# Kernel tuning notes

Measured on AMD Instinct MI355X. Metric: run time of the kernel, lower is better.

Reference implementation:

```python
import jax, jax.numpy as jnp
import numpy as np

B, C, S = 2048, 128, 10          # nodes, channels, species
DIN = 9                           # irreps dim of 0e+1o+2e
DOUTS = (1, 3, 5)                 # dims of output irreps 0e, 1o, 2e
PATHS = (1, 3, 8)                 # num CG paths per correlation order 1..3


def _sparse_normal(key, shape, density=0.15):
    kv, km = jax.random.split(key)
    v = jax.random.normal(kv, shape, jnp.float32)
    m = jax.random.uniform(km, shape) < density
    return jnp.where(m, v, 0.0)


def setup_inputs() -> dict:
    key = jax.random.key(0)
    ks = jax.random.split(key, 11)
    node_feats = jax.random.normal(ks[0], (B, C, DIN), jnp.float32)
    species = jax.random.randint(ks[1], (B,), 0, S)
    node_attrs = jax.nn.one_hot(species, S, dtype=jnp.float32)
    sc = jax.random.normal(ks[2], (B, C * DIN), jnp.float32)
    # CG "U" buffers, stacked over the 3 output irreps, d_out padded to 5.
    U1 = _sparse_normal(ks[3], (3, 5, DIN, PATHS[0]))
    U2 = _sparse_normal(ks[4], (3, 5, DIN, DIN, PATHS[1]))
    U3 = _sparse_normal(ks[5], (3, 5, DIN, DIN, DIN, PATHS[2]))
    # per-species path weights [l_out, species, paths, channels]
    W1 = jax.random.normal(ks[6], (3, S, PATHS[0], C), jnp.float32)
    W2 = jax.random.normal(ks[7], (3, S, PATHS[1], C), jnp.float32)
    W3 = jax.random.normal(ks[8], (3, S, PATHS[2], C), jnp.float32)
    # e3nn Linear: block-diagonal channel mixing per output irrep
    Wlin = jax.random.normal(ks[9], (3, C, C), jnp.float32)
    return dict(node_feats=node_feats, node_attrs=node_attrs, sc=sc,
                U1=U1, U2=U2, U3=U3, W1=W1, W2=W2, W3=W3, Wlin=Wlin)


def reference(node_feats, node_attrs, sc, U1, U2, U3, W1, W2, W3, Wlin):
    x = node_feats                                  # [B, C, 9]
    inv_sqrt_c = 1.0 / np.sqrt(C).astype(np.float32)
    outs = []
    for l, d in enumerate(DOUTS):                   # structural loop over output irreps
        # per-node, per-species weights: [B, P, C]
        w3 = jnp.einsum('be,epc->bpc', node_attrs, W3[l])
        w2 = jnp.einsum('be,epc->bpc', node_attrs, W2[l])
        w1 = jnp.einsum('be,epc->bpc', node_attrs, W1[l])
        u3, u2, u1 = U3[l, :d], U2[l, :d], U1[l, :d]
        # MACE recursive symmetric contraction (highest order first)
        out = jnp.einsum('mijkp,bpc,bck->bcmij', u3, w3, x)   # [B,C,d,9,9]
        out = out + jnp.einsum('mijp,bpc->bcmij', u2, w2)
        out = jnp.einsum('bcmij,bcj->bcmi', out, x)           # [B,C,d,9]
        out = out + jnp.einsum('mip,bpc->bcmi', u1, w1)
        out = jnp.einsum('bcmi,bci->bcm', out, x)             # [B,C,d]
        # axis_to_mul + e3nn Linear (per-irrep channel mixing, element path norm)
        y = jnp.einsum('bcm,cd->bdm', out, Wlin[l]) * inv_sqrt_c
        outs.append(y.reshape(y.shape[0], -1))                # [B, C*d]
    return jnp.concatenate(outs, axis=-1) + sc                # [B, 1152]
```

## Files before the change

kernel.cpp:

```cpp
#include <hip/hip_runtime.h>


#define NB 2048
#define NC 128
#define NS 10

__host__ __device__ constexpr int pidx(int j, int k) {
    return 9 * j - j * (j - 1) / 2 + (k - j);
}

struct TripTab {
    int ti[165], tj[165], tk[165];
    constexpr TripTab() : ti{}, tj{}, tk{} {
        int n = 0;
        for (int i = 0; i < 9; i++)
            for (int j = i; j < 9; j++)
                for (int k = j; k < 9; k++) { ti[n] = i; tj[n] = j; tk[n] = k; n++; }
    }
};
static constexpr TripTab TT{};

struct PairTab {
    int pj[45], pk[45];
    constexpr PairTab() : pj{}, pk{} {
        int n = 0;
        for (int j = 0; j < 9; j++)
            for (int k = j; k < 9; k++) { pj[n] = j; pk[n] = k; n++; }
    }
};
static constexpr PairTab PT{};

__global__ __launch_bounds__(256) void prep_kernel(const float* __restrict__ attrs,
                                                   int* __restrict__ cnt,
                                                   int* __restrict__ start,
                                                   int* __restrict__ list)
{
    __shared__ int sc_[256][NS];
    __shared__ int own_[256][NS];
    __shared__ int st_[NS];
    const int t = threadIdx.x;
    int myspec[8];
    #pragma unroll
    for (int e = 0; e < NS; e++) own_[t][e] = 0;
    #pragma unroll
    for (int r = 0; r < 8; r++) {
        const int b = t * 8 + r;
        const float* row = attrs + b * NS;
        int e = 0;
        #pragma unroll
        for (int s = 1; s < NS; s++) e = (row[s] > 0.5f) ? s : e;
        myspec[r] = e;
        own_[t][e] += 1;
    }
    #pragma unroll
    for (int e = 0; e < NS; e++) sc_[t][e] = own_[t][e];
    __syncthreads();
    for (int off = 1; off < 256; off <<= 1) {
        int tmp[NS];
        #pragma unroll
        for (int e = 0; e < NS; e++) tmp[e] = (t >= off) ? sc_[t - off][e] : 0;
        __syncthreads();
        #pragma unroll
        for (int e = 0; e < NS; e++) sc_[t][e] += tmp[e];
        __syncthreads();
    }
    if (t == 0) {
        int run = 0;
        for (int e = 0; e < NS; e++) {
            st_[e] = run; start[e] = run; cnt[e] = sc_[255][e]; run += sc_[255][e];
        }
    }
    __syncthreads();
    #pragma unroll
    for (int r = 0; r < 8; r++) {
        const int e = myspec[r];
        int rank = 0;
        #pragma unroll
        for (int r2 = 0; r2 < r; r2++) rank += (myspec[r2] == e) ? 1 : 0;
        const int pos = st_[e] + (sc_[t][e] - own_[t][e]) + rank;
        list[pos] = t * 8 + r;
    }
}

__global__ __launch_bounds__(256) void sym_kernel(const float* __restrict__ U2,
                                                  const float* __restrict__ U3,
                                                  float* __restrict__ U3sym,
                                                  float* __restrict__ U2sym)
{
    const int lm = blockIdx.x;
    const int t = threadIdx.x;
    if (t < 165) {
        const int i = TT.ti[t], j = TT.tj[t], k = TT.tk[t];
        const bool eab = (i == j), ebc = (j == k);
        float s[8] = {0, 0, 0, 0, 0, 0, 0, 0};
        auto addp = [&](int a, int b, int c) {
            const float* q = U3 + (((size_t)lm * 729) + a * 81 + b * 9 + c) * 8;
            #pragma unroll
            for (int p = 0; p < 8; p++) s[p] += q[p];
        };
        addp(i, j, k);
        if (!ebc)          addp(i, k, j);
        if (!eab)          addp(j, i, k);
        if (!eab)          addp(j, k, i);
        if (!ebc)          addp(k, i, j);
        if (!(eab || ebc)) addp(k, j, i);
        float* o = U3sym + ((size_t)lm * 165 + t) * 8;
        #pragma unroll
        for (int p = 0; p < 8; p++) o[p] = s[p];
    } else if (t < 210) {
        const int pp = t - 165;
        const int j = PT.pj[pp], k = PT.pk[pp];
        const float* a = U2 + ((size_t)lm * 81 + j * 9 + k) * 3;
        float v0 = a[0], v1 = a[1], v2 = a[2];
        if (j != k) {
            const float* b2 = U2 + ((size_t)lm * 81 + k * 9 + j) * 3;
            v0 += b2[0]; v1 += b2[1]; v2 += b2[2];
        }
        float* o = U2sym + ((size_t)lm * 45 + pp) * 3;
        o[0] = v0; o[1] = v1; o[2] = v2;
    }
}

__global__ __launch_bounds__(256) void main_kernel(
    const float* __restrict__ x_in,
    const float* __restrict__ U1,
    const float* __restrict__ U3sym, const float* __restrict__ U2sym,
    const float* __restrict__ W1, const float* __restrict__ W2, const float* __restrict__ W3,
    const int* __restrict__ cnt, const int* __restrict__ start, const int* __restrict__ list,
    float* __restrict__ inter)
{
    const int c = blockIdx.x;
    const int e = blockIdx.y;
    const int count = cnt[e];
    const int sbase = start[e];

    __shared__ __align__(16) float stab[9 * 660];
    __shared__ float w3s[3][8];
    __shared__ float w2s[3][3];
    __shared__ float w1s[3];

    const int t = threadIdx.x;
    if (t < 24)      { int l = t / 8, p = t % 8; w3s[l][p] = W3[((l * NS + e) * 8 + p) * NC + c]; }
    else if (t < 33) { int q = t - 24; int l = q / 3, p = q % 3; w2s[l][p] = W2[((l * NS + e) * 3 + p) * NC + c]; }
    else if (t < 36) { int l = t - 33; w1s[l] = W1[(l * NS + e) * NC + c]; }
    __syncthreads();

    {
        const int TB[9] = {0, 45, 81, 109, 130, 145, 155, 161, 164};
        for (int n = t; n < 495; n += 256) {
            const int mm = n / 55;
            const int s = n - mm * 55;
            int l, lm;
            if (mm == 0) { l = 0; lm = 0; } else if (mm < 4) { l = 1; lm = 4 + mm; } else { l = 2; lm = 6 + mm; }
            float* tb = stab + mm * 660;
            if (s < 45) {
                const int i = PT.pj[s], j = PT.pk[s];
                const int jj = j - i;
                const int t0 = TB[i] + (9 - i) * jj - jj * (jj - 1) / 2;
                for (int u = 0; u < 12; u++) {
                    float val = 0.f;
                    if (u < 9 - j) {
                        const float* a = U3sym + ((size_t)lm * 165 + t0 + u) * 8;
                        const float4 A = *(const float4*)a;
                        const float4 Bv = *(const float4*)(a + 4);
                        val = A.x * w3s[l][0];
                        val = fmaf(A.y,  w3s[l][1], val);
                        val = fmaf(A.z,  w3s[l][2], val);
                        val = fmaf(A.w,  w3s[l][3], val);
                        val = fmaf(Bv.x, w3s[l][4], val);
                        val = fmaf(Bv.y, w3s[l][5], val);
                        val = fmaf(Bv.z, w3s[l][6], val);
                        val = fmaf(Bv.w, w3s[l][7], val);
                    }
                    tb[s * 12 + u] = val;
                }
            } else if (s < 54) {
                const int j = s - 45;
                for (int u = 0; u < 12; u++) {
                    float val = 0.f;
                    if (u < 9 - j) {
                        const int pp = pidx(j, j + u);
                        const float* a = U2sym + ((size_t)lm * 45 + pp) * 3;
                        val = fmaf(a[0], w2s[l][0], fmaf(a[1], w2s[l][1], a[2] * w2s[l][2]));
                    }
                    tb[540 + j * 12 + u] = val;
                }
            } else {
                for (int u = 0; u < 12; u++) {
                    float val = (u < 9) ? U1[lm * 9 + u] * w1s[l] : 0.f;
                    tb[648 + u] = val;
                }
            }
        }
    }
    __syncthreads();

    #pragma unroll 1
    for (int idx = t; idx < count; idx += 256) {
        const int slot = sbase + idx;
        const int b = list[slot];
        const float* xp = x_in + ((size_t)b * NC + c) * 9;
        float x[9];
        #pragma unroll
        for (int k = 0; k < 9; k++) x[k] = xp[k];

        float* op = inter + ((size_t)c * NB + slot) * 12;

        #pragma unroll 1
        for (int mm = 0; mm < 9; mm++) {
            const float* bp = stab + mm * 660;
            float acc = 0.f;
            #pragma unroll
            for (int i = 0; i < 9; i++) {
                float acci = 0.f;
                #pragma unroll
                for (int j = i; j < 9; j++) {
                    const float* r = bp + pidx(i, j) * 12;
                    const int L = 9 - j;
                    const float4 q0 = *(const float4*)r;
                    float inner = q0.x * x[j];
                    if (L > 1) inner = fmaf(q0.y, x[j + 1], inner);
                    if (L > 2) inner = fmaf(q0.z, x[j + 2], inner);
                    if (L > 3) inner = fmaf(q0.w, x[j + 3], inner);
                    if (L > 4) {
                        const float4 q1 = *(const float4*)(r + 4);
                        inner = fmaf(q1.x, x[j + 4], inner);
                        if (L > 5) inner = fmaf(q1.y, x[j + 5], inner);
                        if (L > 6) inner = fmaf(q1.z, x[j + 6], inner);
                        if (L > 7) inner = fmaf(q1.w, x[j + 7], inner);
                        if (L > 8) {
                            const float4 q2 = *(const float4*)(r + 8);
                            inner = fmaf(q2.x, x[j + 8], inner);
                        }
                    }
                    acci = fmaf(x[j], inner, acci);
                }
                acc = fmaf(x[i], acci, acc);
            }
            #pragma unroll
            for (int j = 0; j < 9; j++) {
                const float* r = bp + 540 + j * 12;
                const int L = 9 - j;
                const float4 q0 = *(const float4*)r;
                float inner = q0.x * x[j];
                if (L > 1) inner = fmaf(q0.y, x[j + 1], inner);
                if (L > 2) inner = fmaf(q0.z, x[j + 2], inner);
                if (L > 3) inner = fmaf(q0.w, x[j + 3], inner);
                if (L > 4) {
                    const float4 q1 = *(const float4*)(r + 4);
                    inner = fmaf(q1.x, x[j + 4], inner);
                    if (L > 5) inner = fmaf(q1.y, x[j + 5], inner);
                    if (L > 6) inner = fmaf(q1.z, x[j + 6], inner);
                    if (L > 7) inner = fmaf(q1.w, x[j + 7], inner);
                    if (L > 8) {
                        const float4 q2 = *(const float4*)(r + 8);
                        inner = fmaf(q2.x, x[j + 8], inner);
                    }
                }
                acc = fmaf(x[j], inner, acc);
            }
            {
                const float* r = bp + 648;
                const float4 q0 = *(const float4*)r;
                const float4 q1 = *(const float4*)(r + 4);
                float inner = q0.x * x[0];
                inner = fmaf(q0.y, x[1], inner);
                inner = fmaf(q0.z, x[2], inner);
                inner = fmaf(q0.w, x[3], inner);
                inner = fmaf(q1.x, x[4], inner);
                inner = fmaf(q1.y, x[5], inner);
                inner = fmaf(q1.z, x[6], inner);
                inner = fmaf(q1.w, x[7], inner);
                inner = fmaf(r[8], x[8], inner);
                acc += inner;
            }
            op[mm] = acc;
        }
    }
}

__global__ __launch_bounds__(256) void final_kernel(
    const float* __restrict__ inter, const float* __restrict__ Wlin,
    const float* __restrict__ sc, const int* __restrict__ list,
    float* __restrict__ out)
{
    __shared__ float sInter[4 * NC * 12];
    const int t = threadIdx.x;
    const int s0 = blockIdx.x * 4;
    #pragma unroll
    for (int q = 0; q < 6; q++) {
        const int flat = t + q * 256;
        const int q3 = flat % 3;
        const int cs = flat / 3;
        const int cc = cs >> 2, s = cs & 3;
        const float4 v = *(const float4*)(inter + ((size_t)cc * NB + s0 + s) * 12 + q3 * 4);
        *(float4*)(&sInter[(s * NC + cc) * 12 + q3 * 4]) = v;
    }
    __syncthreads();

    const int dd = t & 127;
    const int bh = t >> 7;
    float acc[2][9];
    #pragma unroll
    for (int u = 0; u < 2; u++)
        #pragma unroll
        for (int mm = 0; mm < 9; mm++) acc[u][mm] = 0.f;

    const float* wp = Wlin + dd;
    for (int cc = 0; cc < NC; cc++) {
        const float wl0 = wp[(0 * NC + cc) * NC];
        const float wl1 = wp[(1 * NC + cc) * NC];
        const float wl2 = wp[(2 * NC + cc) * NC];
        #pragma unroll
        for (int u = 0; u < 2; u++) {
            const float* ip = sInter + ((bh + u * 2) * NC + cc) * 12;
            const float4 i0 = *(const float4*)ip;
            const float4 i1 = *(const float4*)(ip + 4);
            const float  i8 = ip[8];
            acc[u][0] = fmaf(i0.x, wl0, acc[u][0]);
            acc[u][1] = fmaf(i0.y, wl1, acc[u][1]);
            acc[u][2] = fmaf(i0.z, wl1, acc[u][2]);
            acc[u][3] = fmaf(i0.w, wl1, acc[u][3]);
            acc[u][4] = fmaf(i1.x, wl2, acc[u][4]);
            acc[u][5] = fmaf(i1.y, wl2, acc[u][5]);
            acc[u][6] = fmaf(i1.z, wl2, acc[u][6]);
            acc[u][7] = fmaf(i1.w, wl2, acc[u][7]);
            acc[u][8] = fmaf(i8,   wl2, acc[u][8]);
        }
    }

    const float inv = 0.08838834764831845f;
    #pragma unroll
    for (int u = 0; u < 2; u++) {
        const int s = s0 + bh + u * 2;
        const int b = list[s];
        float* orow = out + (size_t)b * 1152;
        const float* scrow = sc + (size_t)b * 1152;
        orow[dd] = fmaf(acc[u][0], inv, scrow[dd]);
        #pragma unroll
        for (int m = 0; m < 3; m++)
            orow[128 + dd * 3 + m] = fmaf(acc[u][1 + m], inv, scrow[128 + dd * 3 + m]);
        #pragma unroll
        for (int m = 0; m < 5; m++)
            orow[512 + dd * 5 + m] = fmaf(acc[u][4 + m], inv, scrow[512 + dd * 5 + m]);
    }
}

extern "C" void kernel_launch(void* const* d_in, const int* in_sizes, int n_in,
                              void* d_out, int out_size, void* d_ws, size_t ws_size,
                              hipStream_t stream) {
    const float* node_feats = (const float*)d_in[0];
    const float* node_attrs = (const float*)d_in[1];
    const float* sc   = (const float*)d_in[2];
    const float* U1   = (const float*)d_in[3];
    const float* U2   = (const float*)d_in[4];
    const float* U3   = (const float*)d_in[5];
    const float* W1   = (const float*)d_in[6];
    const float* W2   = (const float*)d_in[7];
    const float* W3   = (const float*)d_in[8];
    const float* Wlin = (const float*)d_in[9];
    float* out = (float*)d_out;

    char* ws = (char*)d_ws;
    int* cnt     = (int*)(ws + 0);
    int* start   = (int*)(ws + 64);
    int* list    = (int*)(ws + 128);
    float* U3sym = (float*)(ws + 16384);
    float* U2sym = (float*)(ws + 98304);
    float* inter = (float*)(ws + 131072);

    hipLaunchKernelGGL(prep_kernel, dim3(1), dim3(256), 0, stream,
                       node_attrs, cnt, start, list);
    hipLaunchKernelGGL(sym_kernel, dim3(15), dim3(256), 0, stream,
                       U2, U3, U3sym, U2sym);
    hipLaunchKernelGGL(main_kernel, dim3(NC, NS), dim3(256), 0, stream,
                       node_feats, U1, U3sym, U2sym, W1, W2, W3, cnt, start, list, inter);
    hipLaunchKernelGGL(final_kernel, dim3(NB / 4), dim3(256), 0, stream,
                       inter, Wlin, sc, list, out);
}
```

Baseline: 95.71 us.

## Merge prep and sym kernels; process two nodes per thread in main kernel

The species-bucketing prep kernel and the CG symmetrization kernel are merged into one launch, with block 0 doing the bucketing and blocks 1-15 doing symmetrization, which removes one kernel launch and its serialization. The main kernel drops to 128 threads per block, and each thread now evaluates two nodes at once, so every LDS load of the weighted-U table feeds two FMA chains. This halves shared-memory read traffic per FLOP and adds instruction-level parallelism. The cost is higher register pressure from two x vectors and two sets of accumulators, and fewer threads per block for the table build and latency hiding.

```diff
diff --git a/kernel.cpp b/kernel.cpp
--- a/kernel.cpp
+++ b/kernel.cpp
@@ -30,98 +30,94 @@
 };
 static constexpr PairTab PT{};
 
-__global__ __launch_bounds__(256) void prep_kernel(const float* __restrict__ attrs,
-                                                   int* __restrict__ cnt,
-                                                   int* __restrict__ start,
-                                                   int* __restrict__ list)
+__global__ __launch_bounds__(256) void setup_kernel(
+    const float* __restrict__ attrs,
+    const float* __restrict__ U2, const float* __restrict__ U3,
+    int* __restrict__ cnt, int* __restrict__ start, int* __restrict__ list,
+    float* __restrict__ U3sym, float* __restrict__ U2sym)
 {
-    __shared__ int sc_[256][NS];
-    __shared__ int own_[256][NS];
-    __shared__ int st_[NS];
     const int t = threadIdx.x;
-    int myspec[8];
-    #pragma unroll
-    for (int e = 0; e < NS; e++) own_[t][e] = 0;
-    #pragma unroll
-    for (int r = 0; r < 8; r++) {
-        const int b = t * 8 + r;
-        const float* row = attrs + b * NS;
-        int e = 0;
-        #pragma unroll
-        for (int s = 1; s < NS; s++) e = (row[s] > 0.5f) ? s : e;
-        myspec[r] = e;
-        own_[t][e] += 1;
-    }
-    #pragma unroll
-    for (int e = 0; e < NS; e++) sc_[t][e] = own_[t][e];
-    __syncthreads();
-    for (int off = 1; off < 256; off <<= 1) {
-        int tmp[NS];
-        #pragma unroll
-        for (int e = 0; e < NS; e++) tmp[e] = (t >= off) ? sc_[t - off][e] : 0;
+    if (blockIdx.x == 0) {
+        __shared__ int sc_[256][NS];
+        __shared__ int own_[256][NS];
+        __shared__ int st_[NS];
+        int myspec[8];
+        #pragma unroll
+        for (int e = 0; e < NS; e++) own_[t][e] = 0;
+        #pragma unroll
+        for (int r = 0; r < 8; r++) {
+            const int b = t * 8 + r;
+            const float* row = attrs + b * NS;
+            int e = 0;
+            #pragma unroll
+            for (int s = 1; s < NS; s++) e = (row[s] > 0.5f) ? s : e;
+            myspec[r] = e;
+            own_[t][e] += 1;
+        }
+        #pragma unroll
+        for (int e = 0; e < NS; e++) sc_[t][e] = own_[t][e];
         __syncthreads();
-        #pragma unroll
-        for (int e = 0; e < NS; e++) sc_[t][e] += tmp[e];
+        for (int off = 1; off < 256; off <<= 1) {
+            int tmp[NS];
+            #pragma unroll
+            for (int e = 0; e < NS; e++) tmp[e] = (t >= off) ? sc_[t - off][e] : 0;
+            __syncthreads();
+            #pragma unroll
+            for (int e = 0; e < NS; e++) sc_[t][e] += tmp[e];
+            __syncthreads();
+        }
+        if (t == 0) {
+            int run = 0;
+            for (int e = 0; e < NS; e++) {
+                st_[e] = run; start[e] = run; cnt[e] = sc_[255][e]; run += sc_[255][e];
+            }
+        }
         __syncthreads();
-    }
-    if (t == 0) {
-        int run = 0;
-        for (int e = 0; e < NS; e++) {
-            st_[e] = run; start[e] = run; cnt[e] = sc_[255][e]; run += sc_[255][e];
-        }
-    }
-    __syncthreads();
-    #pragma unroll
-    for (int r = 0; r < 8; r++) {
-        const int e = myspec[r];
-        int rank = 0;
-        #pragma unroll
-        for (int r2 = 0; r2 < r; r2++) rank += (myspec[r2] == e) ? 1 : 0;
-        const int pos = st_[e] + (sc_[t][e] - own_[t][e]) + rank;
-        list[pos] = t * 8 + r;
-    }
-}
-
-__global__ __launch_bounds__(256) void sym_kernel(const float* __restrict__ U2,
-                                                  const float* __restrict__ U3,
-                                                  float* __restrict__ U3sym,
-                                                  float* __restrict__ U2sym)
-{
-    const int lm = blockIdx.x;
-    const int t = threadIdx.x;
-    if (t < 165) {
-        const int i = TT.ti[t], j = TT.tj[t], k = TT.tk[t];
-        const bool eab = (i == j), ebc = (j == k);
-        float s[8] = {0, 0, 0, 0, 0, 0, 0, 0};
-        auto addp = [&](int a, int b, int c) {
-            const float* q = U3 + (((size_t)lm * 729) + a * 81 + b * 9 + c) * 8;
-            #pragma unroll
-            for (int p = 0; p < 8; p++) s[p] += q[p];
-        };
-        addp(i, j, k);
-        if (!ebc)          addp(i, k, j);
-        if (!eab)          addp(j, i, k);
-        if (!eab)          addp(j, k, i);
-        if (!ebc)          addp(k, i, j);
-        if (!(eab || ebc)) addp(k, j, i);
-        float* o = U3sym + ((size_t)lm * 165 + t) * 8;
-        #pragma unroll
-        for (int p = 0; p < 8; p++) o[p] = s[p];
-    } else if (t < 210) {
-        const int pp = t - 165;
-        const int j = PT.pj[pp], k = PT.pk[pp];
-        const float* a = U2 + ((size_t)lm * 81 + j * 9 + k) * 3;
-        float v0 = a[0], v1 = a[1], v2 = a[2];
-        if (j != k) {
-            const float* b2 = U2 + ((size_t)lm * 81 + k * 9 + j) * 3;
-            v0 += b2[0]; v1 += b2[1]; v2 += b2[2];
-        }
-        float* o = U2sym + ((size_t)lm * 45 + pp) * 3;
-        o[0] = v0; o[1] = v1; o[2] = v2;
-    }
-}
-
-__global__ __launch_bounds__(256) void main_kernel(
+        #pragma unroll
+        for (int r = 0; r < 8; r++) {
+            const int e = myspec[r];
+            int rank = 0;
+            #pragma unroll
+            for (int r2 = 0; r2 < r; r2++) rank += (myspec[r2] == e) ? 1 : 0;
+            const int pos = st_[e] + (sc_[t][e] - own_[t][e]) + rank;
+            list[pos] = t * 8 + r;
+        }
+    } else {
+        const int lm = blockIdx.x - 1;
+        if (t < 165) {
+            const int i = TT.ti[t], j = TT.tj[t], k = TT.tk[t];
+            const bool eab = (i == j), ebc = (j == k);
+            float s[8] = {0, 0, 0, 0, 0, 0, 0, 0};
+            auto addp = [&](int a, int b, int c) {
+                const float* q = U3 + (((size_t)lm * 729) + a * 81 + b * 9 + c) * 8;
+                #pragma unroll
+                for (int p = 0; p < 8; p++) s[p] += q[p];
+            };
+            addp(i, j, k);
+            if (!ebc)          addp(i, k, j);
+            if (!eab)          addp(j, i, k);
+            if (!eab)          addp(j, k, i);
+            if (!ebc)          addp(k, i, j);
+            if (!(eab || ebc)) addp(k, j, i);
+            float* o = U3sym + ((size_t)lm * 165 + t) * 8;
+            #pragma unroll
+            for (int p = 0; p < 8; p++) o[p] = s[p];
+        } else if (t < 210) {
+            const int pp = t - 165;
+            const int j = PT.pj[pp], k = PT.pk[pp];
+            const float* a = U2 + ((size_t)lm * 81 + j * 9 + k) * 3;
+            float v0 = a[0], v1 = a[1], v2 = a[2];
+            if (j != k) {
+                const float* b2 = U2 + ((size_t)lm * 81 + k * 9 + j) * 3;
+                v0 += b2[0]; v1 += b2[1]; v2 += b2[2];
+            }
+            float* o = U2sym + ((size_t)lm * 45 + pp) * 3;
+            o[0] = v0; o[1] = v1; o[2] = v2;
+        }
+    }
+}
+
+__global__ __launch_bounds__(128) void main_kernel(
     const float* __restrict__ x_in,
     const float* __restrict__ U1,
     const float* __restrict__ U3sym, const float* __restrict__ U2sym,
@@ -147,7 +143,7 @@
 
     {
         const int TB[9] = {0, 45, 81, 109, 130, 145, 155, 161, 164};
-        for (int n = t; n < 495; n += 256) {
+        for (int n = t; n < 495; n += 128) {
             const int mm = n / 55;
             const int s = n - mm * 55;
             int l, lm;
@@ -196,85 +192,103 @@
     __syncthreads();
 
     #pragma unroll 1
-    for (int idx = t; idx < count; idx += 256) {
-        const int slot = sbase + idx;
-        const int b = list[slot];
-        const float* xp = x_in + ((size_t)b * NC + c) * 9;
-        float x[9];
-        #pragma unroll
-        for (int k = 0; k < 9; k++) x[k] = xp[k];
-
-        float* op = inter + ((size_t)c * NB + slot) * 12;
+    for (int base = 0; base < count; base += 256) {
+        const int ia0 = base + t;
+        const int ia1 = base + t + 128;
+        const bool act0 = ia0 < count;
+        const bool act1 = ia1 < count;
+        const int slot0 = sbase + (act0 ? ia0 : 0);
+        const int slot1 = sbase + (act1 ? ia1 : 0);
+        const int b0 = list[slot0];
+        const int b1 = list[slot1];
+
+        float xa[9], xb[9];
+        const float* xpa = x_in + ((size_t)b0 * NC + c) * 9;
+        const float* xpb = x_in + ((size_t)b1 * NC + c) * 9;
+        #pragma unroll
+        for (int k = 0; k < 9; k++) { xa[k] = xpa[k]; xb[k] = xpb[k]; }
+
+        float* op0 = inter + ((size_t)c * NB + slot0) * 12;
+        float* op1 = inter + ((size_t)c * NB + slot1) * 12;
 
         #pragma unroll 1
         for (int mm = 0; mm < 9; mm++) {
             const float* bp = stab + mm * 660;
-            float acc = 0.f;
+            float acc_a = 0.f, acc_b = 0.f;
             #pragma unroll
             for (int i = 0; i < 9; i++) {
-                float acci = 0.f;
+                float acci_a = 0.f, acci_b = 0.f;
                 #pragma unroll
                 for (int j = i; j < 9; j++) {
                     const float* r = bp + pidx(i, j) * 12;
                     const int L = 9 - j;
                     const float4 q0 = *(const float4*)r;
-                    float inner = q0.x * x[j];
-                    if (L > 1) inner = fmaf(q0.y, x[j + 1], inner);
-                    if (L > 2) inner = fmaf(q0.z, x[j + 2], inner);
-                    if (L > 3) inner = fmaf(q0.w, x[j + 3], inner);
+                    float in_a = q0.x * xa[j];
+                    float in_b = q0.x * xb[j];
+                    if (L > 1) { in_a = fmaf(q0.y, xa[j + 1], in_a); in_b = fmaf(q0.y, xb[j + 1], in_b); }
+                    if (L > 2) { in_a = fmaf(q0.z, xa[j + 2], in_a); in_b = fmaf(q0.z, xb[j + 2], in_b); }
+                    if (L > 3) { in_a = fmaf(q0.w, xa[j + 3], in_a); in_b = fmaf(q0.w, xb[j + 3], in_b); }
                     if (L > 4) {
                         const float4 q1 = *(const float4*)(r + 4);
-                        inner = fmaf(q1.x, x[j + 4], inner);
-                        if (L > 5) inner = fmaf(q1.y, x[j + 5], inner);
-                        if (L > 6) inner = fmaf(q1.z, x[j + 6], inner);
-                        if (L > 7) inner = fmaf(q1.w, x[j + 7], inner);
+                        in_a = fmaf(q1.x, xa[j + 4], in_a); in_b = fmaf(q1.x, xb[j + 4], in_b);
+                        if (L > 5) { in_a = fmaf(q1.y, xa[j + 5], in_a); in_b = fmaf(q1.y, xb[j + 5], in_b); }
+                        if (L > 6) { in_a = fmaf(q1.z, xa[j + 6], in_a); in_b = fmaf(q1.z, xb[j + 6], in_b); }
+                        if (L > 7) { in_a = fmaf(q1.w, xa[j + 7], in_a); in_b = fmaf(q1.w, xb[j + 7], in_b); }
                         if (L > 8) {
-                            const float4 q2 = *(const float4*)(r + 8);
-                            inner = fmaf(q2.x, x[j + 8], inner);
+                            const float q2 = r[8];
+                            in_a = fmaf(q2, xa[j + 8], in_a); in_b = fmaf(q2, xb[j + 8], in_b);
                         }
                     }
-                    acci = fmaf(x[j], inner, acci);
-                }
-                acc = fmaf(x[i], acci, acc);
+                    acci_a = fmaf(xa[j], in_a, acci_a);
+                    acci_b = fmaf(xb[j], in_b, acci_b);
+                }
+                acc_a = fmaf(xa[i], acci_a, acc_a);
+                acc_b = fmaf(xb[i], acci_b, acc_b);
             }
             #pragma unroll
             for (int j = 0; j < 9; j++) {
                 const float* r = bp + 540 + j * 12;
                 const int L = 9 - j;
                 const float4 q0 = *(const float4*)r;
-                float inner = q0.x * x[j];
-                if (L > 1) inner = fmaf(q0.y, x[j + 1], inner);
-                if (L > 2) inner = fmaf(q0.z, x[j + 2], inner);
-                if (L > 3) inner = fmaf(q0.w, x[j + 3], inner);
+                float in_a = q0.x * xa[j];
+                float in_b = q0.x * xb[j];
+                if (L > 1) { in_a = fmaf(q0.y, xa[j + 1], in_a); in_b = fmaf(q0.y, xb[j + 1], in_b); }
+                if (L > 2) { in_a = fmaf(q0.z, xa[j + 2], in_a); in_b = fmaf(q0.z, xb[j + 2], in_b); }
+                if (L > 3) { in_a = fmaf(q0.w, xa[j + 3], in_a); in_b = fmaf(q0.w, xb[j + 3], in_b); }
                 if (L > 4) {
                     const float4 q1 = *(const float4*)(r + 4);
-                    inner = fmaf(q1.x, x[j + 4], inner);
-                    if (L > 5) inner = fmaf(q1.y, x[j + 5], inner);
-                    if (L > 6) inner = fmaf(q1.z, x[j + 6], inner);
-                    if (L > 7) inner = fmaf(q1.w, x[j + 7], inner);
+                    in_a = fmaf(q1.x, xa[j + 4], in_a); in_b = fmaf(q1.x, xb[j + 4], in_b);
+                    if (L > 5) { in_a = fmaf(q1.y, xa[j + 5], in_a); in_b = fmaf(q1.y, xb[j + 5], in_b); }
+                    if (L > 6) { in_a = fmaf(q1.z, xa[j + 6], in_a); in_b = fmaf(q1.z, xb[j + 6], in_b); }
+                    if (L > 7) { in_a = fmaf(q1.w, xa[j + 7], in_a); in_b = fmaf(q1.w, xb[j + 7], in_b); }
                     if (L > 8) {
-                        const float4 q2 = *(const float4*)(r + 8);
-                        inner = fmaf(q2.x, x[j + 8], inner);
+                        const float q2 = r[8];
+                        in_a = fmaf(q2, xa[j + 8], in_a); in_b = fmaf(q2, xb[j + 8], in_b);
                     }
                 }
-                acc = fmaf(x[j], inner, acc);
+                acc_a = fmaf(xa[j], in_a, acc_a);
+                acc_b = fmaf(xb[j], in_b, acc_b);
             }
             {
                 const float* r = bp + 648;
                 const float4 q0 = *(const float4*)r;
                 const float4 q1 = *(const float4*)(r + 4);
-                float inner = q0.x * x[0];
-                inner = fmaf(q0.y, x[1], inner);
-                inner = fmaf(q0.z, x[2], inner);
-                inner = fmaf(q0.w, x[3], inner);
-                inner = fmaf(q1.x, x[4], inner);
-                inner = fmaf(q1.y, x[5], inner);
-                inner = fmaf(q1.z, x[6], inner);
-                inner = fmaf(q1.w, x[7], inner);
-                inner = fmaf(r[8], x[8], inner);
-                acc += inner;
-            }
-            op[mm] = acc;
+                const float r8 = r[8];
+                float in_a = q0.x * xa[0];
+                float in_b = q0.x * xb[0];
+                in_a = fmaf(q0.y, xa[1], in_a); in_b = fmaf(q0.y, xb[1], in_b);
+                in_a = fmaf(q0.z, xa[2], in_a); in_b = fmaf(q0.z, xb[2], in_b);
+                in_a = fmaf(q0.w, xa[3], in_a); in_b = fmaf(q0.w, xb[3], in_b);
+                in_a = fmaf(q1.x, xa[4], in_a); in_b = fmaf(q1.x, xb[4], in_b);
+                in_a = fmaf(q1.y, xa[5], in_a); in_b = fmaf(q1.y, xb[5], in_b);
+                in_a = fmaf(q1.z, xa[6], in_a); in_b = fmaf(q1.z, xb[6], in_b);
+                in_a = fmaf(q1.w, xa[7], in_a); in_b = fmaf(q1.w, xb[7], in_b);
+                in_a = fmaf(r8,   xa[8], in_a); in_b = fmaf(r8,   xb[8], in_b);
+                acc_a += in_a;
+                acc_b += in_b;
+            }
+            if (act0) op0[mm] = acc_a;
+            if (act1) op1[mm] = acc_b;
         }
     }
 }
@@ -369,11 +383,9 @@
     float* U2sym = (float*)(ws + 98304);
     float* inter = (float*)(ws + 131072);
 
-    hipLaunchKernelGGL(prep_kernel, dim3(1), dim3(256), 0, stream,
-                       node_attrs, cnt, start, list);
-    hipLaunchKernelGGL(sym_kernel, dim3(15), dim3(256), 0, stream,
-                       U2, U3, U3sym, U2sym);
-    hipLaunchKernelGGL(main_kernel, dim3(NC, NS), dim3(256), 0, stream,
+    hipLaunchKernelGGL(setup_kernel, dim3(16), dim3(256), 0, stream,
+                       node_attrs, U2, U3, cnt, start, list, U3sym, U2sym);
+    hipLaunchKernelGGL(main_kernel, dim3(NC, NS), dim3(128), 0, stream,
                        node_feats, U1, U3sym, U2sym, W1, W2, W3, cnt, start, list, inter);
     hipLaunchKernelGGL(final_kernel, dim3(NB / 4), dim3(256), 0, stream,
                        inter, Wlin, sc, list, out);
```

Result: slower. 122.4 us (+27.9%).

## Precompute per-species-channel contraction tables in a fused setup kernel

Applied to the files above, without the earlier changes.

Merges the prep and symmetrization kernels into one setup kernel, which builds each (species, channel) weighted contraction table directly from U and W and writes it to global memory. The table layout is compacted to variable row widths. The main kernel then reads these tables from global memory instead of rebuilding them in shared memory per block, which removes a kernel launch and the per-block table construction plus its barrier. In exchange it writes and re-reads about 14.5 MB of tables through global memory and cache, and the setup kernel repeats the 6-permutation symmetrization work for every channel.

```diff
diff --git a/kernel.cpp b/kernel.cpp
--- a/kernel.cpp
+++ b/kernel.cpp
@@ -4,21 +4,25 @@
 #define NB 2048
 #define NC 128
 #define NS 10
+#define TMM 316
+#define TROW (9 * TMM)
 
 __host__ __device__ constexpr int pidx(int j, int k) {
     return 9 * j - j * (j - 1) / 2 + (k - j);
 }
-
-struct TripTab {
-    int ti[165], tj[165], tk[165];
-    constexpr TripTab() : ti{}, tj{}, tk{} {
-        int n = 0;
+__host__ __device__ constexpr int wj(int j) { int L = 9 - j; return L <= 4 ? 4 : (L <= 8 ? 8 : 12); }
+
+struct OffTab {
+    int s3[45]; int s2[9]; int s1;
+    constexpr OffTab() : s3{}, s2{}, s1(0) {
+        int o = 0;
         for (int i = 0; i < 9; i++)
-            for (int j = i; j < 9; j++)
-                for (int k = j; k < 9; k++) { ti[n] = i; tj[n] = j; tk[n] = k; n++; }
+            for (int j = i; j < 9; j++) { s3[pidx(i, j)] = o; o += wj(j); }
+        for (int j = 0; j < 9; j++) { s2[j] = o; o += wj(j); }
+        s1 = o;
     }
 };
-static constexpr TripTab TT{};
+static constexpr OffTab OT{};
 
 struct PairTab {
     int pj[45], pk[45];
@@ -30,102 +34,141 @@
 };
 static constexpr PairTab PT{};
 
-__global__ __launch_bounds__(256) void prep_kernel(const float* __restrict__ attrs,
-                                                   int* __restrict__ cnt,
-                                                   int* __restrict__ start,
-                                                   int* __restrict__ list)
+__global__ __launch_bounds__(256) void setup_kernel(
+    const float* __restrict__ attrs,
+    const float* __restrict__ U1, const float* __restrict__ U2, const float* __restrict__ U3,
+    const float* __restrict__ W1, const float* __restrict__ W2, const float* __restrict__ W3,
+    int* __restrict__ cnt, int* __restrict__ start, int* __restrict__ list,
+    float* __restrict__ tabs)
 {
-    __shared__ int sc_[256][NS];
-    __shared__ int own_[256][NS];
-    __shared__ int st_[NS];
     const int t = threadIdx.x;
-    int myspec[8];
-    #pragma unroll
-    for (int e = 0; e < NS; e++) own_[t][e] = 0;
-    #pragma unroll
-    for (int r = 0; r < 8; r++) {
-        const int b = t * 8 + r;
-        const float* row = attrs + b * NS;
-        int e = 0;
-        #pragma unroll
-        for (int s = 1; s < NS; s++) e = (row[s] > 0.5f) ? s : e;
-        myspec[r] = e;
-        own_[t][e] += 1;
-    }
-    #pragma unroll
-    for (int e = 0; e < NS; e++) sc_[t][e] = own_[t][e];
-    __syncthreads();
-    for (int off = 1; off < 256; off <<= 1) {
-        int tmp[NS];
-        #pragma unroll
-        for (int e = 0; e < NS; e++) tmp[e] = (t >= off) ? sc_[t - off][e] : 0;
+    if (blockIdx.x == 0) {
+        __shared__ int sc_[256][NS];
+        __shared__ int own_[256][NS];
+        __shared__ int st_[NS];
+        int myspec[8];
+        #pragma unroll
+        for (int e = 0; e < NS; e++) own_[t][e] = 0;
+        #pragma unroll
+        for (int r = 0; r < 8; r++) {
+            const int b = t * 8 + r;
+            const float* row = attrs + b * NS;
+            int e = 0;
+            #pragma unroll
+            for (int s = 1; s < NS; s++) e = (row[s] > 0.5f) ? s : e;
+            myspec[r] = e;
+            own_[t][e] += 1;
+        }
+        #pragma unroll
+        for (int e = 0; e < NS; e++) sc_[t][e] = own_[t][e];
         __syncthreads();
-        #pragma unroll
-        for (int e = 0; e < NS; e++) sc_[t][e] += tmp[e];
+        for (int off = 1; off < 256; off <<= 1) {
+            int tmp[NS];
+            #pragma unroll
+            for (int e = 0; e < NS; e++) tmp[e] = (t >= off) ? sc_[t - off][e] : 0;
+            __syncthreads();
+            #pragma unroll
+            for (int e = 0; e < NS; e++) sc_[t][e] += tmp[e];
+            __syncthreads();
+        }
+        if (t == 0) {
+            int run = 0;
+            for (int e = 0; e < NS; e++) {
+                st_[e] = run; start[e] = run; cnt[e] = sc_[255][e]; run += sc_[255][e];
+            }
+        }
         __syncthreads();
-    }
-    if (t == 0) {
-        int run = 0;
-        for (int e = 0; e < NS; e++) {
-            st_[e] = run; start[e] = run; cnt[e] = sc_[255][e]; run += sc_[255][e];
-        }
-    }
-    __syncthreads();
-    #pragma unroll
-    for (int r = 0; r < 8; r++) {
-        const int e = myspec[r];
-        int rank = 0;
-        #pragma unroll
-        for (int r2 = 0; r2 < r; r2++) rank += (myspec[r2] == e) ? 1 : 0;
-        const int pos = st_[e] + (sc_[t][e] - own_[t][e]) + rank;
-        list[pos] = t * 8 + r;
-    }
-}
-
-__global__ __launch_bounds__(256) void sym_kernel(const float* __restrict__ U2,
-                                                  const float* __restrict__ U3,
-                                                  float* __restrict__ U3sym,
-                                                  float* __restrict__ U2sym)
-{
-    const int lm = blockIdx.x;
-    const int t = threadIdx.x;
-    if (t < 165) {
-        const int i = TT.ti[t], j = TT.tj[t], k = TT.tk[t];
-        const bool eab = (i == j), ebc = (j == k);
-        float s[8] = {0, 0, 0, 0, 0, 0, 0, 0};
-        auto addp = [&](int a, int b, int c) {
-            const float* q = U3 + (((size_t)lm * 729) + a * 81 + b * 9 + c) * 8;
-            #pragma unroll
-            for (int p = 0; p < 8; p++) s[p] += q[p];
-        };
-        addp(i, j, k);
-        if (!ebc)          addp(i, k, j);
-        if (!eab)          addp(j, i, k);
-        if (!eab)          addp(j, k, i);
-        if (!ebc)          addp(k, i, j);
-        if (!(eab || ebc)) addp(k, j, i);
-        float* o = U3sym + ((size_t)lm * 165 + t) * 8;
-        #pragma unroll
-        for (int p = 0; p < 8; p++) o[p] = s[p];
-    } else if (t < 210) {
-        const int pp = t - 165;
-        const int j = PT.pj[pp], k = PT.pk[pp];
-        const float* a = U2 + ((size_t)lm * 81 + j * 9 + k) * 3;
-        float v0 = a[0], v1 = a[1], v2 = a[2];
-        if (j != k) {
-            const float* b2 = U2 + ((size_t)lm * 81 + k * 9 + j) * 3;
-            v0 += b2[0]; v1 += b2[1]; v2 += b2[2];
-        }
-        float* o = U2sym + ((size_t)lm * 45 + pp) * 3;
-        o[0] = v0; o[1] = v1; o[2] = v2;
+        #pragma unroll
+        for (int r = 0; r < 8; r++) {
+            const int e = myspec[r];
+            int rank = 0;
+            #pragma unroll
+            for (int r2 = 0; r2 < r; r2++) rank += (myspec[r2] == e) ? 1 : 0;
+            const int pos = st_[e] + (sc_[t][e] - own_[t][e]) + rank;
+            list[pos] = t * 8 + r;
+        }
+    } else {
+        const int n1 = blockIdx.x - 1;
+        const int e = n1 / NC;
+        const int c = n1 - e * NC;
+
+        __shared__ float w3s[3][8];
+        __shared__ float w2s[3][3];
+        __shared__ float w1s[3];
+        if (t < 24)      { int l = t / 8, p = t % 8; w3s[l][p] = W3[((l * NS + e) * 8 + p) * NC + c]; }
+        else if (t < 33) { int q = t - 24; int l = q / 3, p = q % 3; w2s[l][p] = W2[((l * NS + e) * 3 + p) * NC + c]; }
+        else if (t < 36) { int l = t - 33; w1s[l] = W1[(l * NS + e) * NC + c]; }
+        __syncthreads();
+
+        float* tab = tabs + (size_t)n1 * TROW;
+        for (int n = t; n < 9 * 55; n += 256) {
+            const int mm = n / 55;
+            const int s = n - mm * 55;
+            int l, lm;
+            if (mm == 0) { l = 0; lm = 0; } else if (mm < 4) { l = 1; lm = 4 + mm; } else { l = 2; lm = 6 + mm; }
+            float* sec = tab + mm * TMM;
+            if (s < 45) {
+                const int i = PT.pj[s], j = PT.pk[s];
+                const int W = wj(j);
+                float* dst = sec + OT.s3[s];
+                for (int u = 0; u < W; u++) {
+                    float val = 0.f;
+                    const int k = j + u;
+                    if (u < 9 - j) {
+                        const bool eab = (i == j), ebc = (j == k);
+                        float sum = 0.f;
+                        auto addp = [&](int a, int b2, int c2) {
+                            const float4* q = (const float4*)(U3 + (((size_t)lm * 729) + a * 81 + b2 * 9 + c2) * 8);
+                            const float4 A = q[0], Bv = q[1];
+                            float av = A.x * w3s[l][0];
+                            av = fmaf(A.y,  w3s[l][1], av);
+                            av = fmaf(A.z,  w3s[l][2], av);
+                            av = fmaf(A.w,  w3s[l][3], av);
+                            av = fmaf(Bv.x, w3s[l][4], av);
+                            av = fmaf(Bv.y, w3s[l][5], av);
+                            av = fmaf(Bv.z, w3s[l][6], av);
+                            av = fmaf(Bv.w, w3s[l][7], av);
+                            sum += av;
+                        };
+                        addp(i, j, k);
+                        if (!ebc)          addp(i, k, j);
+                        if (!eab)          addp(j, i, k);
+                        if (!eab)          addp(j, k, i);
+                        if (!ebc)          addp(k, i, j);
+                        if (!(eab || ebc)) addp(k, j, i);
+                        val = sum;
+                    }
+                    dst[u] = val;
+                }
+            } else if (s < 54) {
+                const int j = s - 45;
+                const int W = wj(j);
+                float* dst = sec + OT.s2[j];
+                for (int u = 0; u < W; u++) {
+                    float val = 0.f;
+                    const int k = j + u;
+                    if (u < 9 - j) {
+                        const float* a = U2 + ((size_t)lm * 81 + j * 9 + k) * 3;
+                        val = fmaf(a[0], w2s[l][0], fmaf(a[1], w2s[l][1], a[2] * w2s[l][2]));
+                        if (j != k) {
+                            const float* b2 = U2 + ((size_t)lm * 81 + k * 9 + j) * 3;
+                            val = fmaf(b2[0], w2s[l][0], fmaf(b2[1], w2s[l][1], fmaf(b2[2], w2s[l][2], val)));
+                        }
+                    }
+                    dst[u] = val;
+                }
+            } else {
+                float* dst = sec + OT.s1;
+                for (int u = 0; u < 12; u++)
+                    dst[u] = (u < 9) ? U1[lm * 9 + u] * w1s[l] : 0.f;
+            }
+        }
     }
 }
 
 __global__ __launch_bounds__(256) void main_kernel(
     const float* __restrict__ x_in,
-    const float* __restrict__ U1,
-    const float* __restrict__ U3sym, const float* __restrict__ U2sym,
-    const float* __restrict__ W1, const float* __restrict__ W2, const float* __restrict__ W3,
+    const float* __restrict__ tabs,
     const int* __restrict__ cnt, const int* __restrict__ start, const int* __restrict__ list,
     float* __restrict__ inter)
 {
@@ -133,67 +176,9 @@
     const int e = blockIdx.y;
     const int count = cnt[e];
     const int sbase = start[e];
-
-    __shared__ __align__(16) float stab[9 * 660];
-    __shared__ float w3s[3][8];
-    __shared__ float w2s[3][3];
-    __shared__ float w1s[3];
+    const float* tab = tabs + (size_t)(e * NC + c) * TROW;
 
     const int t = threadIdx.x;
-    if (t < 24)      { int l = t / 8, p = t % 8; w3s[l][p] = W3[((l * NS + e) * 8 + p) * NC + c]; }
-    else if (t < 33) { int q = t - 24; int l = q / 3, p = q % 3; w2s[l][p] = W2[((l * NS + e) * 3 + p) * NC + c]; }
-    else if (t < 36) { int l = t - 33; w1s[l] = W1[(l * NS + e) * NC + c]; }
-    __syncthreads();
-
-    {
-        const int TB[9] = {0, 45, 81, 109, 130, 145, 155, 161, 164};
-        for (int n = t; n < 495; n += 256) {
-            const int mm = n / 55;
-            const int s = n - mm * 55;
-            int l, lm;
-            if (mm == 0) { l = 0; lm = 0; } else if (mm < 4) { l = 1; lm = 4 + mm; } else { l = 2; lm = 6 + mm; }
-            float* tb = stab + mm * 660;
-            if (s < 45) {
-                const int i = PT.pj[s], j = PT.pk[s];
-                const int jj = j - i;
-                const int t0 = TB[i] + (9 - i) * jj - jj * (jj - 1) / 2;
-                for (int u = 0; u < 12; u++) {
-                    float val = 0.f;
-                    if (u < 9 - j) {
-                        const float* a = U3sym + ((size_t)lm * 165 + t0 + u) * 8;
-                        const float4 A = *(const float4*)a;
-                        const float4 Bv = *(const float4*)(a + 4);
-                        val = A.x * w3s[l][0];
-                        val = fmaf(A.y,  w3s[l][1], val);
-                        val = fmaf(A.z,  w3s[l][2], val);
-                        val = fmaf(A.w,  w3s[l][3], val);
-                        val = fmaf(Bv.x, w3s[l][4], val);
-                        val = fmaf(Bv.y, w3s[l][5], val);
-                        val = fmaf(Bv.z, w3s[l][6], val);
-                        val = fmaf(Bv.w, w3s[l][7], val);
-                    }
-                    tb[s * 12 + u] = val;
-                }
-            } else if (s < 54) {
-                const int j = s - 45;
-                for (int u = 0; u < 12; u++) {
-                    float val = 0.f;
-                    if (u < 9 - j) {
-                        const int pp = pidx(j, j + u);
-                        const float* a = U2sym + ((size_t)lm * 45 + pp) * 3;
-                        val = fmaf(a[0], w2s[l][0], fmaf(a[1], w2s[l][1], a[2] * w2s[l][2]));
-                    }
-                    tb[540 + j * 12 + u] = val;
-                }
-            } else {
-                for (int u = 0; u < 12; u++) {
-                    float val = (u < 9) ? U1[lm * 9 + u] * w1s[l] : 0.f;
-                    tb[648 + u] = val;
-                }
-            }
-        }
-    }
-    __syncthreads();
 
     #pragma unroll 1
     for (int idx = t; idx < count; idx += 256) {
@@ -208,14 +193,14 @@
 
         #pragma unroll 1
         for (int mm = 0; mm < 9; mm++) {
-            const float* bp = stab + mm * 660;
+            const float* bp = tab + mm * TMM;
             float acc = 0.f;
             #pragma unroll
             for (int i = 0; i < 9; i++) {
                 float acci = 0.f;
                 #pragma unroll
                 for (int j = i; j < 9; j++) {
-                    const float* r = bp + pidx(i, j) * 12;
+                    const float* r = bp + OT.s3[pidx(i, j)];
                     const int L = 9 - j;
                     const float4 q0 = *(const float4*)r;
                     float inner = q0.x * x[j];
@@ -239,7 +224,7 @@
             }
             #pragma unroll
             for (int j = 0; j < 9; j++) {
-                const float* r = bp + 540 + j * 12;
+                const float* r = bp + OT.s2[j];
                 const int L = 9 - j;
                 const float4 q0 = *(const float4*)r;
                 float inner = q0.x * x[j];
@@ -260,7 +245,7 @@
                 acc = fmaf(x[j], inner, acc);
             }
             {
-                const float* r = bp + 648;
+                const float* r = bp + OT.s1;
                 const float4 q0 = *(const float4*)r;
                 const float4 q1 = *(const float4*)(r + 4);
                 float inner = q0.x * x[0];
@@ -365,16 +350,13 @@
     int* cnt     = (int*)(ws + 0);
     int* start   = (int*)(ws + 64);
     int* list    = (int*)(ws + 128);
-    float* U3sym = (float*)(ws + 16384);
-    float* U2sym = (float*)(ws + 98304);
-    float* inter = (float*)(ws + 131072);
-
-    hipLaunchKernelGGL(prep_kernel, dim3(1), dim3(256), 0, stream,
-                       node_attrs, cnt, start, list);
-    hipLaunchKernelGGL(sym_kernel, dim3(15), dim3(256), 0, stream,
-                       U2, U3, U3sym, U2sym);
+    float* tabs  = (float*)(ws + 16384);
+    float* inter = (float*)(ws + 16384 + 14561280);
+
+    hipLaunchKernelGGL(setup_kernel, dim3(1 + NC * NS), dim3(256), 0, stream,
+                       node_attrs, U1, U2, U3, W1, W2, W3, cnt, start, list, tabs);
     hipLaunchKernelGGL(main_kernel, dim3(NC, NS), dim3(256), 0, stream,
-                       node_feats, U1, U3sym, U2sym, W1, W2, W3, cnt, start, list, inter);
+                       node_feats, tabs, cnt, start, list, inter);
     hipLaunchKernelGGL(final_kernel, dim3(NB / 4), dim3(256), 0, stream,
                        inter, Wlin, sc, list, out);
 }
```

Result: slower. 128.0 us (+33.7%).
